# Performance work log

Hardware: AMD Instinct MI355X
Metric: run time of the kernel (lower is better)

## Reference

```python
import jax, jax.numpy as jnp
import numpy as np
import math

B, S, H = 2, 4096, 512
NUM_HEADS = 8
HEAD_DIM = H // NUM_HEADS
RECENCY_DECAY = 0.9


def setup_inputs() -> dict:
    key = jax.random.key(0)
    k1, k2, k3 = jax.random.split(key, 3)
    scale = 1.0 / math.sqrt(H)
    x = jax.random.normal(k1, (B, S, H), dtype=jnp.float32)
    w_qkv = jax.random.normal(k2, (3 * H, H), dtype=jnp.float32) * scale
    w_out = jax.random.normal(k3, (H, H), dtype=jnp.float32) * scale
    b_out = jnp.zeros((H,), dtype=jnp.float32)
    return {"x": x, "w_qkv": w_qkv, "w_out": w_out, "b_out": b_out}


def reference(x, w_qkv, w_out, b_out):
    batch, seq_len, hidden = x.shape
    nh, hd = NUM_HEADS, HEAD_DIM
    # qkv projection (no bias): torch Linear computes x @ W.T
    qkv = jnp.einsum('bsh,oh->bso', x, w_qkv)
    qkv = qkv.reshape(batch, seq_len, 3, nh, hd)
    q, k, v = jnp.transpose(qkv, (2, 0, 3, 1, 4))  # each [B, nh, S, hd]
    attn = jnp.einsum('bhqd,bhkd->bhqk', q, k) / math.sqrt(hd)
    # recency bias: positions[i, j] = j - i; bias = (j-i)*log(decay) for j<=i else 0
    pos = jnp.arange(seq_len)[None, :] - jnp.arange(seq_len)[:, None]
    bias = jnp.where(pos <= 0, pos.astype(jnp.float32) * math.log(RECENCY_DECAY),
                     jnp.zeros((), dtype=jnp.float32))
    attn = jax.nn.softmax(attn + bias[None, None, :, :], axis=-1)
    out = jnp.einsum('bhqk,bhkd->bqhd', attn, v).reshape(batch, seq_len, hidden)
    return jnp.einsum('bsh,oh->bso', out, w_out) + b_out
```

## Files before the change

### kernel.cpp

```cpp
#include <hip/hip_runtime.h>
#include <hip/hip_bf16.h>
#include <stdint.h>

#define B_   2
#define S_   4096
#define H_   512
#define NH_  8
#define HD_  64
#define M_   (B_*S_)
#define LOG2D (-0.15200309344504997f)
#define SC2   (0.18033688011112042f)

#define NFULL        4
#define NCHUNK       8

typedef __attribute__((ext_vector_type(8))) short bf16x8_t;
typedef __attribute__((ext_vector_type(4))) float f32x4_t;

__device__ __forceinline__ void gl_lds16(const __hip_bfloat16* g, __hip_bfloat16* l) {
  __builtin_amdgcn_global_load_lds(
      (__attribute__((address_space(1))) void*)(g),
      (__attribute__((address_space(3))) void*)(l),
      16, 0, 0);
}

__global__ __launch_bounds__(256)
void cast3_kernel(const float* __restrict__ x, const float* __restrict__ wq,
                  const float* __restrict__ wo,
                  __hip_bfloat16* __restrict__ xb, __hip_bfloat16* __restrict__ wqb,
                  __hip_bfloat16* __restrict__ wob) {
  const int N0 = M_ * H_;
  const int N1 = 3 * H_ * H_;
  int i4 = (blockIdx.x * blockDim.x + threadIdx.x) * 4;
  const float* src; __hip_bfloat16* dst; int off;
  if (i4 < N0)           { src = x;  dst = xb;  off = i4; }
  else if (i4 < N0 + N1) { src = wq; dst = wqb; off = i4 - N0; }
  else                   { src = wo; dst = wob; off = i4 - N0 - N1; }
  float4 v = *(const float4*)(src + off);
  ushort4 o;
  __hip_bfloat16 h;
  h = __float2bfloat16(v.x); o.x = *(unsigned short*)&h;
  h = __float2bfloat16(v.y); o.y = *(unsigned short*)&h;
  h = __float2bfloat16(v.z); o.z = *(unsigned short*)&h;
  h = __float2bfloat16(v.w); o.w = *(unsigned short*)&h;
  *(ushort4*)((unsigned short*)dst + off) = o;
}

template<int EPI>
__global__ __launch_bounds__(256)
void gemm_bt(const __hip_bfloat16* __restrict__ A,
             const __hip_bfloat16* __restrict__ Bw,
             int K,
             __hip_bfloat16* __restrict__ qb,
             __hip_bfloat16* __restrict__ kb,
             __hip_bfloat16* __restrict__ vtb,
             float* __restrict__ outp,
             const float* __restrict__ bias) {
  __shared__ alignas(16) __hip_bfloat16 sA[128*64];
  __shared__ alignas(16) __hip_bfloat16 sB[128*64];
  const int tid  = threadIdx.x;
  const int wave = tid >> 6, lane = tid & 63;
  const int quad = lane >> 4, l15 = lane & 15;
  const int wr = (wave >> 1) * 64, wc = (wave & 1) * 64;
  const int m0 = blockIdx.y * 128, n0 = blockIdx.x * 128;

  const int sub  = lane >> 3;
  const int plog = (lane & 7) ^ sub;

  f32x4_t acc[4][4] = {};

  for (int kt = 0; kt < K; kt += 64) {
    __syncthreads();
    #pragma unroll
    for (int cc = 0; cc < 4; cc++) {
      int c   = wave * 4 + cc;
      int row = c * 8 + sub;
      gl_lds16(A  + (size_t)(m0 + row) * K + kt + plog * 8, sA + c * 512);
      gl_lds16(Bw + (size_t)(n0 + row) * K + kt + plog * 8, sB + c * 512);
    }
    __syncthreads();
    #pragma unroll
    for (int kh = 0; kh < 2; kh++) {
      bf16x8_t af[4], bfr[4];
      #pragma unroll
      for (int x = 0; x < 4; x++) {
        int row = wr + x * 16 + l15;
        int pos = kh * 4 + quad;
        af[x] = *(const bf16x8_t*)(sA + row * 64 + ((pos ^ (row & 7)) << 3));
      }
      #pragma unroll
      for (int y = 0; y < 4; y++) {
        int row = wc + y * 16 + l15;
        int pos = kh * 4 + quad;
        bfr[y] = *(const bf16x8_t*)(sB + row * 64 + ((pos ^ (row & 7)) << 3));
      }
      #pragma unroll
      for (int x = 0; x < 4; x++)
        #pragma unroll
        for (int y = 0; y < 4; y++)
          acc[x][y] = __builtin_amdgcn_mfma_f32_16x16x32_bf16(af[x], bfr[y], acc[x][y], 0, 0, 0);
    }
  }

  #pragma unroll
  for (int x = 0; x < 4; x++) {
    #pragma unroll
    for (int y = 0; y < 4; y++) {
      #pragma unroll
      for (int r = 0; r < 4; r++) {
        int gr = m0 + wr + x*16 + quad*4 + r;
        int gc = n0 + wc + y*16 + l15;
        float v = acc[x][y][r];
        if (EPI == 0) {
          int bb = gr >> 12, s = gr & 4095;
          int t  = gc >> 9,  rem = gc & 511;
          int h  = rem >> 6, d = rem & 63;
          __hip_bfloat16 hv = __float2bfloat16(v);
          int bh = bb * NH_ + h;
          if (t == 0)      qb [((size_t)bh * S_ + s) * HD_ + d] = hv;
          else if (t == 1) kb [((size_t)bh * S_ + s) * HD_ + d] = hv;
          else             vtb[((size_t)bh * HD_ + d) * S_ + s] = hv;
        } else {
          outp[(size_t)gr * H_ + gc] = v + bias[gc];
        }
      }
    }
  }
}

__device__ __forceinline__ void stage_kv(const __hip_bfloat16* __restrict__ kb,
                                         const __hip_bfloat16* __restrict__ vtb,
                                         int bh, int j0,
                                         __hip_bfloat16* dK, __hip_bfloat16* dV,
                                         int wave, int lane) {
  const int subK  = lane >> 3;
  const int plogK = (lane & 7) ^ subK;
  const int subV  = lane >> 4;
  #pragma unroll
  for (int cc = 0; cc < 4; cc++) {
    int c = wave * 4 + cc;
    int rK = c * 8 + subK;
    gl_lds16(kb + ((size_t)bh * S_ + j0 + rK) * HD_ + plogK * 8, dK + c * 512);
    int rV = c * 4 + subV;
    int plogV = (lane & 15) ^ (rV & 15);
    gl_lds16(vtb + ((size_t)bh * HD_ + rV) * S_ + j0 + plogV * 8, dV + c * 512);
  }
}

__global__ __launch_bounds__(256)
void attn_kernel(const __hip_bfloat16* __restrict__ qb,
                 const __hip_bfloat16* __restrict__ kb,
                 const __hip_bfloat16* __restrict__ vtb,
                 __hip_bfloat16* __restrict__ ob,
                 float* __restrict__ pO,
                 float* __restrict__ pl) {
  __shared__ alignas(16) __hip_bfloat16 sK[128*64];
  __shared__ alignas(16) __hip_bfloat16 sV[64*128];
  __shared__ alignas(16) __hip_bfloat16 sP[4][16*128];

  const int tid  = threadIdx.x;
  const int wave = tid >> 6, lane = tid & 63;
  const int quad = lane >> 4, l15 = lane & 15;
  const int w  = blockIdx.x;
  const int bh = blockIdx.y;

  int q0, jt0, niter;
  bool direct;
  if (w < 30) { q0 = 256 + w * 128; jt0 = 0; niter = 2; direct = true;  }
  else { int t = w - 30; q0 = (t >> 3) * 128; jt0 = (t & 7) * 4; niter = 4; direct = false; }

  const int rgb0 = q0 + wave * 32;
  bf16x8_t aQ[2][2];
  #pragma unroll
  for (int g = 0; g < 2; g++) {
    const __hip_bfloat16* qrow = qb + ((size_t)bh * S_ + rgb0 + g * 16 + l15) * HD_;
    aQ[g][0] = *(const bf16x8_t*)(qrow + quad * 8);
    aQ[g][1] = *(const bf16x8_t*)(qrow + 32 + quad * 8);
  }

  f32x4_t accO[2][4] = {};
  float l_r[2][4];
  float negM2[2][4];
  #pragma unroll
  for (int g = 0; g < 2; g++)
    #pragma unroll
    for (int r = 0; r < 4; r++) {
      l_r[g][r] = 0.f;
      negM2[g][r] = -(17.312340f - LOG2D * (float)(rgb0 + g * 16 + quad * 4 + r));
    }

  __hip_bfloat16* sPw = &sP[wave][0];

  for (int it = 0; it < niter; ++it) {
    const int j0 = (jt0 + it) * 128;
    __syncthreads();
    stage_kv(kb, vtb, bh, j0, sK, sV, wave, lane);
    __syncthreads();

    #pragma unroll
    for (int g = 0; g < 2; ++g) {
      const int rgb = rgb0 + g * 16;

      f32x4_t sfr[8];
      #pragma unroll
      for (int ni = 0; ni < 8; ni++) {
        int row = ni * 16 + l15;
        f32x4_t a = {};
        bf16x8_t b0 = *(const bf16x8_t*)(sK + row * 64 + ((quad       ^ (row & 7)) << 3));
        bf16x8_t b1 = *(const bf16x8_t*)(sK + row * 64 + (((quad + 4) ^ (row & 7)) << 3));
        a = __builtin_amdgcn_mfma_f32_16x16x32_bf16(aQ[g][0], b0, a, 0, 0, 0);
        a = __builtin_amdgcn_mfma_f32_16x16x32_bf16(aQ[g][1], b1, a, 0, 0, 0);
        sfr[ni] = a;
      }

      const int mode = (j0 + 128 <= rgb) ? 0 : ((j0 >= rgb + 16) ? 1 : 2);
      if (mode == 0) {
        float cj[8];
        #pragma unroll
        for (int ni = 0; ni < 8; ni++)
          cj[ni] = fmaf((float)(j0 + ni * 16 + l15), LOG2D, -17.312340f);
        #pragma unroll
        for (int r = 0; r < 4; r++) {
          const int row = quad * 4 + r;
          float psum = 0.f;
          #pragma unroll
          for (int ni = 0; ni < 8; ni++) {
            float p = __builtin_amdgcn_exp2f(fmaf(sfr[ni][r], SC2, cj[ni]));
            psum += p;
            int col = ni * 16 + l15;
            sPw[row * 128 + (((col >> 3) ^ (row & 15)) << 3) + (col & 7)] = __float2bfloat16(p);
          }
          l_r[g][r] += psum;
        }
      } else if (mode == 1) {
        #pragma unroll
        for (int r = 0; r < 4; r++) {
          const int row = quad * 4 + r;
          float psum = 0.f;
          #pragma unroll
          for (int ni = 0; ni < 8; ni++) {
            float p = __builtin_amdgcn_exp2f(fmaf(sfr[ni][r], SC2, negM2[g][r]));
            psum += p;
            int col = ni * 16 + l15;
            sPw[row * 128 + (((col >> 3) ^ (row & 15)) << 3) + (col & 7)] = __float2bfloat16(p);
          }
          l_r[g][r] += psum;
        }
      } else {
        #pragma unroll
        for (int r = 0; r < 4; r++) {
          const float d0 = (float)(j0 + l15 - (rgb + quad * 4 + r));
          const int row = quad * 4 + r;
          float psum = 0.f;
          #pragma unroll
          for (int ni = 0; ni < 8; ni++) {
            float dij = d0 + (float)(ni * 16);
            float arg = fmaf(fminf(dij, 0.f), LOG2D, fmaf(sfr[ni][r], SC2, negM2[g][r]));
            float p = __builtin_amdgcn_exp2f(arg);
            psum += p;
            int col = ni * 16 + l15;
            sPw[row * 128 + (((col >> 3) ^ (row & 15)) << 3) + (col & 7)] = __float2bfloat16(p);
          }
          l_r[g][r] += psum;
        }
      }
      __builtin_amdgcn_sched_barrier(0);
      __builtin_amdgcn_s_waitcnt(0xC07F);
      __builtin_amdgcn_sched_barrier(0);

      #pragma unroll
      for (int kk = 0; kk < 4; kk++) {
        int pos = kk * 4 + quad;
        bf16x8_t aP = *(const bf16x8_t*)(sPw + l15 * 128 + ((pos ^ l15) << 3));
        #pragma unroll
        for (int nd = 0; nd < 4; nd++) {
          int row = nd * 16 + l15;
          bf16x8_t bV = *(const bf16x8_t*)(sV + row * 128 + ((pos ^ (row & 15)) << 3));
          accO[g][nd] = __builtin_amdgcn_mfma_f32_16x16x32_bf16(aP, bV, accO[g][nd], 0, 0, 0);
        }
      }
      __builtin_amdgcn_sched_barrier(0);
    }
  }

  if (direct) {
    const int b = bh >> 3, h = bh & 7;
    #pragma unroll
    for (int g = 0; g < 2; g++) {
      #pragma unroll
      for (int r = 0; r < 4; r++) {
        float l = l_r[g][r];
        #pragma unroll
        for (int msk = 1; msk < 16; msk <<= 1) l += __shfl_xor(l, msk, 64);
        l_r[g][r] = 1.0f / l;
      }
      #pragma unroll
      for (int nd = 0; nd < 4; nd++)
        #pragma unroll
        for (int r = 0; r < 4; r++) {
          int srow = rgb0 + g * 16 + quad * 4 + r;
          int col  = h * HD_ + nd * 16 + l15;
          ob[((size_t)b * S_ + srow) * H_ + col] = __float2bfloat16(accO[g][nd][r] * l_r[g][r]);
        }
    }
  } else {
    const int qt    = (q0 >> 6) + (wave >> 1);
    const int rbase = (wave & 1) * 32;
    size_t base = ((size_t)bh * NFULL + qt) * NCHUNK + (size_t)(jt0 >> 2);
    float* po = pO + base * 4096;
    #pragma unroll
    for (int g = 0; g < 2; g++) {
      #pragma unroll
      for (int r = 0; r < 4; r++) {
        float l = l_r[g][r];
        #pragma unroll
        for (int msk = 1; msk < 16; msk <<= 1) l += __shfl_xor(l, msk, 64);
        l_r[g][r] = l;
      }
      #pragma unroll
      for (int nd = 0; nd < 4; nd++)
        #pragma unroll
        for (int r = 0; r < 4; r++)
          po[(rbase + g*16 + quad*4 + r) * 64 + nd*16 + l15] = accO[g][nd][r];
      if (l15 == 0) {
        #pragma unroll
        for (int r = 0; r < 4; r++)
          pl[base * 64 + rbase + g*16 + quad*4 + r] = l_r[g][r];
      }
    }
  }
}

__global__ __launch_bounds__(256)
void combine_kernel(const float* __restrict__ pO,
                    const float* __restrict__ pl,
                    __hip_bfloat16* __restrict__ ob) {
  const int f  = blockIdx.x;
  const int bh = blockIdx.y;
  const int tid = threadIdx.x;
  const int rr = tid >> 2, cg = (tid & 3) * 16;
  const size_t base0 = ((size_t)bh * NFULL + f) * NCHUNK;

  float L = 0.f;
  #pragma unroll
  for (int c = 0; c < NCHUNK; c++) L += pl[(base0 + c) * 64 + rr];
  const float inv = 1.0f / L;

  float o[16];
  #pragma unroll
  for (int k = 0; k < 16; k++) o[k] = 0.f;
  #pragma unroll
  for (int c = 0; c < NCHUNK; c++) {
    const float4* src = (const float4*)(pO + (base0 + c) * 4096 + rr * 64 + cg);
    #pragma unroll
    for (int k4 = 0; k4 < 4; k4++) {
      float4 v = src[k4];
      o[k4*4+0] += v.x; o[k4*4+1] += v.y;
      o[k4*4+2] += v.z; o[k4*4+3] += v.w;
    }
  }
  const int b = bh >> 3, h = bh & 7, s = f * 64 + rr;
  __hip_bfloat16* dst = ob + ((size_t)b * S_ + s) * H_ + h * HD_ + cg;
  #pragma unroll
  for (int k = 0; k < 16; k++) dst[k] = __float2bfloat16(o[k] * inv);
}

extern "C" void kernel_launch(void* const* d_in, const int* in_sizes, int n_in,
                              void* d_out, int out_size, void* d_ws, size_t ws_size,
                              hipStream_t stream) {
  const float* x     = (const float*)d_in[0];
  const float* w_qkv = (const float*)d_in[1];
  const float* w_out = (const float*)d_in[2];
  const float* b_out = (const float*)d_in[3];
  float* out = (float*)d_out;

  char* ws = (char*)d_ws;
  __hip_bfloat16* xb  = (__hip_bfloat16*)(ws);
  __hip_bfloat16* wqb = (__hip_bfloat16*)(ws + (8u  << 20));
  __hip_bfloat16* wob = (__hip_bfloat16*)(ws + (10u << 20));
  __hip_bfloat16* qb  = (__hip_bfloat16*)(ws + (11u << 20));
  __hip_bfloat16* kb  = (__hip_bfloat16*)(ws + (19u << 20));
  __hip_bfloat16* vtb = (__hip_bfloat16*)(ws + (27u << 20));
  float*          pO  = (float*)(ws + (36u << 20));
  float*          pl  = (float*)(ws + (49u << 20));
  __hip_bfloat16* ab  = xb;

  cast3_kernel<<<dim3(5120), dim3(256), 0, stream>>>(x, w_qkv, w_out, xb, wqb, wob);
  gemm_bt<0><<<dim3(12, 64), dim3(256), 0, stream>>>(xb, wqb, H_, qb, kb, vtb, nullptr, nullptr);
  attn_kernel<<<dim3(30 + 2 * NCHUNK, B_ * NH_), dim3(256), 0, stream>>>(qb, kb, vtb, ab, pO, pl);
  combine_kernel<<<dim3(NFULL, B_ * NH_), dim3(256), 0, stream>>>(pO, pl, ab);
  gemm_bt<1><<<dim3(4, 64), dim3(256), 0, stream>>>(ab, wob, H_, nullptr, nullptr, nullptr, out, b_out);
}
```

Baseline: 151.6 us.

## Enlarge attention query tile to 256 rows and vectorize V-transpose stores

New measurement: 154.2 us. Within noise of the previous version (+1.7%).

```diff
diff --git a/kernel.cpp b/kernel.cpp
--- a/kernel.cpp
+++ b/kernel.cpp
@@ -102,26 +102,44 @@
     }
   }
 
-  #pragma unroll
-  for (int x = 0; x < 4; x++) {
-    #pragma unroll
-    for (int y = 0; y < 4; y++) {
-      #pragma unroll
-      for (int r = 0; r < 4; r++) {
-        int gr = m0 + wr + x*16 + quad*4 + r;
-        int gc = n0 + wc + y*16 + l15;
-        float v = acc[x][y][r];
-        if (EPI == 0) {
-          int bb = gr >> 12, s = gr & 4095;
-          int t  = gc >> 9,  rem = gc & 511;
-          int h  = rem >> 6, d = rem & 63;
-          __hip_bfloat16 hv = __float2bfloat16(v);
-          int bh = bb * NH_ + h;
-          if (t == 0)      qb [((size_t)bh * S_ + s) * HD_ + d] = hv;
-          else if (t == 1) kb [((size_t)bh * S_ + s) * HD_ + d] = hv;
-          else             vtb[((size_t)bh * HD_ + d) * S_ + s] = hv;
-        } else {
-          outp[(size_t)gr * H_ + gc] = v + bias[gc];
+  if (EPI == 0 && (n0 >> 9) == 2) {
+    #pragma unroll
+    for (int x = 0; x < 4; x++) {
+      int gr = m0 + wr + x * 16 + quad * 4;
+      int bb = gr >> 12, sb = gr & 4095;
+      #pragma unroll
+      for (int y = 0; y < 4; y++) {
+        int rem = (n0 - 1024) + wc + y * 16 + l15;
+        int h = rem >> 6, d = rem & 63;
+        ushort4 o; __hip_bfloat16 hv;
+        hv = __float2bfloat16(acc[x][y][0]); o.x = *(unsigned short*)&hv;
+        hv = __float2bfloat16(acc[x][y][1]); o.y = *(unsigned short*)&hv;
+        hv = __float2bfloat16(acc[x][y][2]); o.z = *(unsigned short*)&hv;
+        hv = __float2bfloat16(acc[x][y][3]); o.w = *(unsigned short*)&hv;
+        *(ushort4*)(vtb + ((size_t)(bb * NH_ + h) * HD_ + d) * S_ + sb) = o;
+      }
+    }
+  } else {
+    #pragma unroll
+    for (int x = 0; x < 4; x++) {
+      #pragma unroll
+      for (int y = 0; y < 4; y++) {
+        #pragma unroll
+        for (int r = 0; r < 4; r++) {
+          int gr = m0 + wr + x*16 + quad*4 + r;
+          int gc = n0 + wc + y*16 + l15;
+          float v = acc[x][y][r];
+          if (EPI == 0) {
+            int bb = gr >> 12, s = gr & 4095;
+            int t  = gc >> 9,  rem = gc & 511;
+            int h  = rem >> 6, d = rem & 63;
+            __hip_bfloat16 hv = __float2bfloat16(v);
+            int bh = bb * NH_ + h;
+            if (t == 0) qb[((size_t)bh * S_ + s) * HD_ + d] = hv;
+            else        kb[((size_t)bh * S_ + s) * HD_ + d] = hv;
+          } else {
+            outp[(size_t)gr * H_ + gc] = v + bias[gc];
+          }
         }
       }
     }
@@ -164,30 +182,34 @@
   const int w  = blockIdx.x;
   const int bh = blockIdx.y;
 
-  int q0, jt0, niter;
+  int q0, jt0, niter, chunk = 0;
   bool direct;
-  if (w < 30) { q0 = 256 + w * 128; jt0 = 0; niter = 2; direct = true;  }
-  else { int t = w - 30; q0 = (t >> 3) * 128; jt0 = (t & 7) * 4; niter = 4; direct = false; }
-
-  const int rgb0 = q0 + wave * 32;
-  bf16x8_t aQ[2][2];
-  #pragma unroll
-  for (int g = 0; g < 2; g++) {
+  if (w < 15) { q0 = 256 + w * 256; jt0 = 0; niter = 2; direct = true; }
+  else { chunk = w - 15; q0 = 0; jt0 = chunk * 4; niter = 4; direct = false; }
+
+  const int rgb0 = q0 + wave * 64;
+  bf16x8_t aQ[4][2];
+  #pragma unroll
+  for (int g = 0; g < 4; g++) {
     const __hip_bfloat16* qrow = qb + ((size_t)bh * S_ + rgb0 + g * 16 + l15) * HD_;
     aQ[g][0] = *(const bf16x8_t*)(qrow + quad * 8);
     aQ[g][1] = *(const bf16x8_t*)(qrow + 32 + quad * 8);
   }
 
-  f32x4_t accO[2][4] = {};
-  float l_r[2][4];
-  float negM2[2][4];
-  #pragma unroll
-  for (int g = 0; g < 2; g++)
-    #pragma unroll
-    for (int r = 0; r < 4; r++) {
-      l_r[g][r] = 0.f;
-      negM2[g][r] = -(17.312340f - LOG2D * (float)(rgb0 + g * 16 + quad * 4 + r));
-    }
+  f32x4_t accO[4][4] = {};
+  float l_r[4][4];
+  float negM2[4][4];
+  #pragma unroll
+  for (int g = 0; g < 4; g++)
+    #pragma unroll
+    for (int r = 0; r < 4; r++) l_r[g][r] = 0.f;
+  if (!direct) {
+    #pragma unroll
+    for (int g = 0; g < 4; g++)
+      #pragma unroll
+      for (int r = 0; r < 4; r++)
+        negM2[g][r] = -(17.312340f - LOG2D * (float)(rgb0 + g * 16 + quad * 4 + r));
+  }
 
   __hip_bfloat16* sPw = &sP[wave][0];
 
@@ -197,8 +219,15 @@
     stage_kv(kb, vtb, bh, j0, sK, sV, wave, lane);
     __syncthreads();
 
-    #pragma unroll
-    for (int g = 0; g < 2; ++g) {
+    float cjd[8];
+    if (direct) {
+      #pragma unroll
+      for (int ni = 0; ni < 8; ni++)
+        cjd[ni] = fmaf((float)(j0 + ni * 16 + l15), LOG2D, -17.312340f);
+    }
+
+    #pragma unroll
+    for (int g = 0; g < 4; ++g) {
       const int rgb = rgb0 + g * 16;
 
       f32x4_t sfr[8];
@@ -213,33 +242,14 @@
         sfr[ni] = a;
       }
 
-      const int mode = (j0 + 128 <= rgb) ? 0 : ((j0 >= rgb + 16) ? 1 : 2);
-      if (mode == 0) {
-        float cj[8];
-        #pragma unroll
-        for (int ni = 0; ni < 8; ni++)
-          cj[ni] = fmaf((float)(j0 + ni * 16 + l15), LOG2D, -17.312340f);
+      if (direct) {
         #pragma unroll
         for (int r = 0; r < 4; r++) {
           const int row = quad * 4 + r;
           float psum = 0.f;
           #pragma unroll
           for (int ni = 0; ni < 8; ni++) {
-            float p = __builtin_amdgcn_exp2f(fmaf(sfr[ni][r], SC2, cj[ni]));
-            psum += p;
-            int col = ni * 16 + l15;
-            sPw[row * 128 + (((col >> 3) ^ (row & 15)) << 3) + (col & 7)] = __float2bfloat16(p);
-          }
-          l_r[g][r] += psum;
-        }
-      } else if (mode == 1) {
-        #pragma unroll
-        for (int r = 0; r < 4; r++) {
-          const int row = quad * 4 + r;
-          float psum = 0.f;
-          #pragma unroll
-          for (int ni = 0; ni < 8; ni++) {
-            float p = __builtin_amdgcn_exp2f(fmaf(sfr[ni][r], SC2, negM2[g][r]));
+            float p = __builtin_amdgcn_exp2f(fmaf(sfr[ni][r], SC2, cjd[ni]));
             psum += p;
             int col = ni * 16 + l15;
             sPw[row * 128 + (((col >> 3) ^ (row & 15)) << 3) + (col & 7)] = __float2bfloat16(p);
@@ -247,21 +257,56 @@
           l_r[g][r] += psum;
         }
       } else {
-        #pragma unroll
-        for (int r = 0; r < 4; r++) {
-          const float d0 = (float)(j0 + l15 - (rgb + quad * 4 + r));
-          const int row = quad * 4 + r;
-          float psum = 0.f;
+        const int mode = (j0 + 128 <= rgb) ? 0 : ((j0 >= rgb + 16) ? 1 : 2);
+        if (mode == 0) {
+          float cj[8];
           #pragma unroll
-          for (int ni = 0; ni < 8; ni++) {
-            float dij = d0 + (float)(ni * 16);
-            float arg = fmaf(fminf(dij, 0.f), LOG2D, fmaf(sfr[ni][r], SC2, negM2[g][r]));
-            float p = __builtin_amdgcn_exp2f(arg);
-            psum += p;
-            int col = ni * 16 + l15;
-            sPw[row * 128 + (((col >> 3) ^ (row & 15)) << 3) + (col & 7)] = __float2bfloat16(p);
+          for (int ni = 0; ni < 8; ni++)
+            cj[ni] = fmaf((float)(j0 + ni * 16 + l15), LOG2D, -17.312340f);
+          #pragma unroll
+          for (int r = 0; r < 4; r++) {
+            const int row = quad * 4 + r;
+            float psum = 0.f;
+            #pragma unroll
+            for (int ni = 0; ni < 8; ni++) {
+              float p = __builtin_amdgcn_exp2f(fmaf(sfr[ni][r], SC2, cj[ni]));
+              psum += p;
+              int col = ni * 16 + l15;
+              sPw[row * 128 + (((col >> 3) ^ (row & 15)) << 3) + (col & 7)] = __float2bfloat16(p);
+            }
+            l_r[g][r] += psum;
           }
-          l_r[g][r] += psum;
+        } else if (mode == 1) {
+          #pragma unroll
+          for (int r = 0; r < 4; r++) {
+            const int row = quad * 4 + r;
+            float psum = 0.f;
+            #pragma unroll
+            for (int ni = 0; ni < 8; ni++) {
+              float p = __builtin_amdgcn_exp2f(fmaf(sfr[ni][r], SC2, negM2[g][r]));
+              psum += p;
+              int col = ni * 16 + l15;
+              sPw[row * 128 + (((col >> 3) ^ (row & 15)) << 3) + (col & 7)] = __float2bfloat16(p);
+            }
+            l_r[g][r] += psum;
+          }
+        } else {
+          #pragma unroll
+          for (int r = 0; r < 4; r++) {
+            const float d0 = (float)(j0 + l15 - (rgb + quad * 4 + r));
+            const int row = quad * 4 + r;
+            float psum = 0.f;
+            #pragma unroll
+            for (int ni = 0; ni < 8; ni++) {
+              float dij = d0 + (float)(ni * 16);
+              float arg = fmaf(fminf(dij, 0.f), LOG2D, fmaf(sfr[ni][r], SC2, negM2[g][r]));
+              float p = __builtin_amdgcn_exp2f(arg);
+              psum += p;
+              int col = ni * 16 + l15;
+              sPw[row * 128 + (((col >> 3) ^ (row & 15)) << 3) + (col & 7)] = __float2bfloat16(p);
+            }
+            l_r[g][r] += psum;
+          }
         }
       }
       __builtin_amdgcn_sched_barrier(0);
@@ -283,49 +328,47 @@
     }
   }
 
+  #pragma unroll
+  for (int g = 0; g < 4; g++)
+    #pragma unroll
+    for (int r = 0; r < 4; r++) {
+      float l = l_r[g][r];
+      #pragma unroll
+      for (int msk = 1; msk < 16; msk <<= 1) l += __shfl_xor(l, msk, 64);
+      l_r[g][r] = l;
+    }
+
   if (direct) {
     const int b = bh >> 3, h = bh & 7;
     #pragma unroll
-    for (int g = 0; g < 2; g++) {
+    for (int g = 0; g < 4; g++) {
+      const float inv = 1.0f / l_r[g][0 + 0];
+      (void)inv;
       #pragma unroll
       for (int r = 0; r < 4; r++) {
-        float l = l_r[g][r];
-        #pragma unroll
-        for (int msk = 1; msk < 16; msk <<= 1) l += __shfl_xor(l, msk, 64);
-        l_r[g][r] = 1.0f / l;
-      }
-      #pragma unroll
-      for (int nd = 0; nd < 4; nd++)
-        #pragma unroll
-        for (int r = 0; r < 4; r++) {
+        float invr = 1.0f / l_r[g][r];
+        #pragma unroll
+        for (int nd = 0; nd < 4; nd++) {
           int srow = rgb0 + g * 16 + quad * 4 + r;
           int col  = h * HD_ + nd * 16 + l15;
-          ob[((size_t)b * S_ + srow) * H_ + col] = __float2bfloat16(accO[g][nd][r] * l_r[g][r]);
+          ob[((size_t)b * S_ + srow) * H_ + col] = __float2bfloat16(accO[g][nd][r] * invr);
         }
+      }
     }
   } else {
-    const int qt    = (q0 >> 6) + (wave >> 1);
-    const int rbase = (wave & 1) * 32;
-    size_t base = ((size_t)bh * NFULL + qt) * NCHUNK + (size_t)(jt0 >> 2);
+    size_t base = ((size_t)bh * NFULL + wave) * NCHUNK + chunk;
     float* po = pO + base * 4096;
     #pragma unroll
-    for (int g = 0; g < 2; g++) {
-      #pragma unroll
-      for (int r = 0; r < 4; r++) {
-        float l = l_r[g][r];
-        #pragma unroll
-        for (int msk = 1; msk < 16; msk <<= 1) l += __shfl_xor(l, msk, 64);
-        l_r[g][r] = l;
-      }
+    for (int g = 0; g < 4; g++) {
       #pragma unroll
       for (int nd = 0; nd < 4; nd++)
         #pragma unroll
         for (int r = 0; r < 4; r++)
-          po[(rbase + g*16 + quad*4 + r) * 64 + nd*16 + l15] = accO[g][nd][r];
+          po[(g*16 + quad*4 + r) * 64 + nd*16 + l15] = accO[g][nd][r];
       if (l15 == 0) {
         #pragma unroll
         for (int r = 0; r < 4; r++)
-          pl[base * 64 + rbase + g*16 + quad*4 + r] = l_r[g][r];
+          pl[base * 64 + g*16 + quad*4 + r] = l_r[g][r];
       }
     }
   }
@@ -387,7 +430,7 @@
 
   cast3_kernel<<<dim3(5120), dim3(256), 0, stream>>>(x, w_qkv, w_out, xb, wqb, wob);
   gemm_bt<0><<<dim3(12, 64), dim3(256), 0, stream>>>(xb, wqb, H_, qb, kb, vtb, nullptr, nullptr);
-  attn_kernel<<<dim3(30 + 2 * NCHUNK, B_ * NH_), dim3(256), 0, stream>>>(qb, kb, vtb, ab, pO, pl);
+  attn_kernel<<<dim3(15 + NCHUNK, B_ * NH_), dim3(256), 0, stream>>>(qb, kb, vtb, ab, pO, pl);
   combine_kernel<<<dim3(NFULL, B_ * NH_), dim3(256), 0, stream>>>(pO, pl, ab);
   gemm_bt<1><<<dim3(4, 64), dim3(256), 0, stream>>>(ab, wob, H_, nullptr, nullptr, nullptr, out, b_out);
 }
```

## Vectorize V-transpose stores in QKV epilogue and unify softmax bias path

Applied to the files above, without the earlier changes.

After: 145.8 us. -3.9%, faster.

```diff
diff --git a/kernel.cpp b/kernel.cpp
--- a/kernel.cpp
+++ b/kernel.cpp
@@ -102,26 +102,44 @@
     }
   }
 
-  #pragma unroll
-  for (int x = 0; x < 4; x++) {
-    #pragma unroll
-    for (int y = 0; y < 4; y++) {
-      #pragma unroll
-      for (int r = 0; r < 4; r++) {
-        int gr = m0 + wr + x*16 + quad*4 + r;
-        int gc = n0 + wc + y*16 + l15;
-        float v = acc[x][y][r];
-        if (EPI == 0) {
-          int bb = gr >> 12, s = gr & 4095;
-          int t  = gc >> 9,  rem = gc & 511;
-          int h  = rem >> 6, d = rem & 63;
-          __hip_bfloat16 hv = __float2bfloat16(v);
-          int bh = bb * NH_ + h;
-          if (t == 0)      qb [((size_t)bh * S_ + s) * HD_ + d] = hv;
-          else if (t == 1) kb [((size_t)bh * S_ + s) * HD_ + d] = hv;
-          else             vtb[((size_t)bh * HD_ + d) * S_ + s] = hv;
-        } else {
-          outp[(size_t)gr * H_ + gc] = v + bias[gc];
+  if (EPI == 0 && (n0 >> 9) == 2) {
+    #pragma unroll
+    for (int x = 0; x < 4; x++) {
+      int gr = m0 + wr + x * 16 + quad * 4;
+      int bb = gr >> 12, sb = gr & 4095;
+      #pragma unroll
+      for (int y = 0; y < 4; y++) {
+        int rem = (n0 - 1024) + wc + y * 16 + l15;
+        int h = rem >> 6, d = rem & 63;
+        ushort4 o; __hip_bfloat16 hv;
+        hv = __float2bfloat16(acc[x][y][0]); o.x = *(unsigned short*)&hv;
+        hv = __float2bfloat16(acc[x][y][1]); o.y = *(unsigned short*)&hv;
+        hv = __float2bfloat16(acc[x][y][2]); o.z = *(unsigned short*)&hv;
+        hv = __float2bfloat16(acc[x][y][3]); o.w = *(unsigned short*)&hv;
+        *(ushort4*)(vtb + ((size_t)(bb * NH_ + h) * HD_ + d) * S_ + sb) = o;
+      }
+    }
+  } else {
+    #pragma unroll
+    for (int x = 0; x < 4; x++) {
+      #pragma unroll
+      for (int y = 0; y < 4; y++) {
+        #pragma unroll
+        for (int r = 0; r < 4; r++) {
+          int gr = m0 + wr + x*16 + quad*4 + r;
+          int gc = n0 + wc + y*16 + l15;
+          float v = acc[x][y][r];
+          if (EPI == 0) {
+            int bb = gr >> 12, s = gr & 4095;
+            int t  = gc >> 9,  rem = gc & 511;
+            int h  = rem >> 6, d = rem & 63;
+            __hip_bfloat16 hv = __float2bfloat16(v);
+            int bh = bb * NH_ + h;
+            if (t == 0) qb[((size_t)bh * S_ + s) * HD_ + d] = hv;
+            else        kb[((size_t)bh * S_ + s) * HD_ + d] = hv;
+          } else {
+            outp[(size_t)gr * H_ + gc] = v + bias[gc];
+          }
         }
       }
     }
@@ -164,10 +182,10 @@
   const int w  = blockIdx.x;
   const int bh = blockIdx.y;
 
-  int q0, jt0, niter;
+  int q0, jt0, niter, chunk = 0;
   bool direct;
-  if (w < 30) { q0 = 256 + w * 128; jt0 = 0; niter = 2; direct = true;  }
-  else { int t = w - 30; q0 = (t >> 3) * 128; jt0 = (t & 7) * 4; niter = 4; direct = false; }
+  if (w < 30) { q0 = 256 + w * 128; jt0 = 0; niter = 2; direct = true; }
+  else { int t = w - 30; chunk = t & 7; q0 = (t >> 3) * 128; jt0 = chunk * 4; niter = 4; direct = false; }
 
   const int rgb0 = q0 + wave * 32;
   bf16x8_t aQ[2][2];
@@ -199,8 +217,6 @@
 
     #pragma unroll
     for (int g = 0; g < 2; ++g) {
-      const int rgb = rgb0 + g * 16;
-
       f32x4_t sfr[8];
       #pragma unroll
       for (int ni = 0; ni < 8; ni++) {
@@ -213,56 +229,21 @@
         sfr[ni] = a;
       }
 
-      const int mode = (j0 + 128 <= rgb) ? 0 : ((j0 >= rgb + 16) ? 1 : 2);
-      if (mode == 0) {
-        float cj[8];
-        #pragma unroll
-        for (int ni = 0; ni < 8; ni++)
-          cj[ni] = fmaf((float)(j0 + ni * 16 + l15), LOG2D, -17.312340f);
-        #pragma unroll
-        for (int r = 0; r < 4; r++) {
-          const int row = quad * 4 + r;
-          float psum = 0.f;
-          #pragma unroll
-          for (int ni = 0; ni < 8; ni++) {
-            float p = __builtin_amdgcn_exp2f(fmaf(sfr[ni][r], SC2, cj[ni]));
-            psum += p;
-            int col = ni * 16 + l15;
-            sPw[row * 128 + (((col >> 3) ^ (row & 15)) << 3) + (col & 7)] = __float2bfloat16(p);
-          }
-          l_r[g][r] += psum;
+      #pragma unroll
+      for (int r = 0; r < 4; r++) {
+        const float d0 = (float)(j0 + l15 - (rgb0 + g * 16 + quad * 4 + r));
+        const int row = quad * 4 + r;
+        float psum = 0.f;
+        #pragma unroll
+        for (int ni = 0; ni < 8; ni++) {
+          float dij = d0 + (float)(ni * 16);
+          float arg = fmaf(fminf(dij, 0.f), LOG2D, fmaf(sfr[ni][r], SC2, negM2[g][r]));
+          float p = __builtin_amdgcn_exp2f(arg);
+          psum += p;
+          int col = ni * 16 + l15;
+          sPw[row * 128 + (((col >> 3) ^ (row & 15)) << 3) + (col & 7)] = __float2bfloat16(p);
         }
-      } else if (mode == 1) {
-        #pragma unroll
-        for (int r = 0; r < 4; r++) {
-          const int row = quad * 4 + r;
-          float psum = 0.f;
-          #pragma unroll
-          for (int ni = 0; ni < 8; ni++) {
-            float p = __builtin_amdgcn_exp2f(fmaf(sfr[ni][r], SC2, negM2[g][r]));
-            psum += p;
-            int col = ni * 16 + l15;
-            sPw[row * 128 + (((col >> 3) ^ (row & 15)) << 3) + (col & 7)] = __float2bfloat16(p);
-          }
-          l_r[g][r] += psum;
-        }
-      } else {
-        #pragma unroll
-        for (int r = 0; r < 4; r++) {
-          const float d0 = (float)(j0 + l15 - (rgb + quad * 4 + r));
-          const int row = quad * 4 + r;
-          float psum = 0.f;
-          #pragma unroll
-          for (int ni = 0; ni < 8; ni++) {
-            float dij = d0 + (float)(ni * 16);
-            float arg = fmaf(fminf(dij, 0.f), LOG2D, fmaf(sfr[ni][r], SC2, negM2[g][r]));
-            float p = __builtin_amdgcn_exp2f(arg);
-            psum += p;
-            int col = ni * 16 + l15;
-            sPw[row * 128 + (((col >> 3) ^ (row & 15)) << 3) + (col & 7)] = __float2bfloat16(p);
-          }
-          l_r[g][r] += psum;
-        }
+        l_r[g][r] += psum;
       }
       __builtin_amdgcn_sched_barrier(0);
       __builtin_amdgcn_s_waitcnt(0xC07F);
@@ -283,40 +264,37 @@
     }
   }
 
+  #pragma unroll
+  for (int g = 0; g < 2; g++)
+    #pragma unroll
+    for (int r = 0; r < 4; r++) {
+      float l = l_r[g][r];
+      #pragma unroll
+      for (int msk = 1; msk < 16; msk <<= 1) l += __shfl_xor(l, msk, 64);
+      l_r[g][r] = l;
+    }
+
   if (direct) {
     const int b = bh >> 3, h = bh & 7;
     #pragma unroll
-    for (int g = 0; g < 2; g++) {
+    for (int g = 0; g < 2; g++)
       #pragma unroll
       for (int r = 0; r < 4; r++) {
-        float l = l_r[g][r];
-        #pragma unroll
-        for (int msk = 1; msk < 16; msk <<= 1) l += __shfl_xor(l, msk, 64);
-        l_r[g][r] = 1.0f / l;
-      }
-      #pragma unroll
-      for (int nd = 0; nd < 4; nd++)
-        #pragma unroll
-        for (int r = 0; r < 4; r++) {
+        float invr = 1.0f / l_r[g][r];
+        #pragma unroll
+        for (int nd = 0; nd < 4; nd++) {
           int srow = rgb0 + g * 16 + quad * 4 + r;
           int col  = h * HD_ + nd * 16 + l15;
-          ob[((size_t)b * S_ + srow) * H_ + col] = __float2bfloat16(accO[g][nd][r] * l_r[g][r]);
+          ob[((size_t)b * S_ + srow) * H_ + col] = __float2bfloat16(accO[g][nd][r] * invr);
         }
-    }
+      }
   } else {
     const int qt    = (q0 >> 6) + (wave >> 1);
     const int rbase = (wave & 1) * 32;
-    size_t base = ((size_t)bh * NFULL + qt) * NCHUNK + (size_t)(jt0 >> 2);
+    size_t base = ((size_t)bh * NFULL + qt) * NCHUNK + chunk;
     float* po = pO + base * 4096;
     #pragma unroll
     for (int g = 0; g < 2; g++) {
-      #pragma unroll
-      for (int r = 0; r < 4; r++) {
-        float l = l_r[g][r];
-        #pragma unroll
-        for (int msk = 1; msk < 16; msk <<= 1) l += __shfl_xor(l, msk, 64);
-        l_r[g][r] = l;
-      }
       #pragma unroll
       for (int nd = 0; nd < 4; nd++)
         #pragma unroll
```
